# Kernel tuning notes

Hardware: AMD Instinct MI355X
Metric: run time of the kernel (lower is better)

The kernel has to match this reference:

```python
import jax, jax.numpy as jnp
import numpy as np

B, S, HID, H = 2, 2048, 1024, 16
D = HID // H  # head dim = 64


def setup_inputs() -> dict:
    key = jax.random.key(0)
    ks = jax.random.split(key, 16)
    scale = 0.02
    inp = {
        "hidden_states": jax.random.normal(ks[0], (B, S, HID), jnp.float32),
        "attention_mask": jnp.zeros((B, 1, 1, S), jnp.float32),
        "hashtag_mask": jax.random.uniform(ks[1], (B, S), jnp.float32),
        "mention_mask": jax.random.uniform(ks[2], (B, S), jnp.float32),
        "emoji_mask": jax.random.uniform(ks[3], (B, S), jnp.float32),
        # Linear weights stored as [in, out] (torch uses [out, in]; math identical via x @ W)
        "Wq": jax.random.normal(ks[4], (HID, HID), jnp.float32) * scale,
        "bq": jnp.zeros((HID,), jnp.float32),
        "Wk": jax.random.normal(ks[5], (HID, HID), jnp.float32) * scale,
        "bk": jnp.zeros((HID,), jnp.float32),
        "Wv": jax.random.normal(ks[6], (HID, HID), jnp.float32) * scale,
        "bv": jnp.zeros((HID,), jnp.float32),
        "Wo": jax.random.normal(ks[7], (HID, HID), jnp.float32) * scale,
        "bo": jnp.zeros((HID,), jnp.float32),
        # per-head scalar social biases [1, H, 1, 1]
        "hashtag_bias": jax.random.normal(ks[8], (1, H, 1, 1), jnp.float32) * 0.1,
        "mention_bias": jax.random.normal(ks[9], (1, H, 1, 1), jnp.float32) * 0.1,
        "emoji_bias": jax.random.normal(ks[10], (1, H, 1, 1), jnp.float32) * 0.1,
    }
    return inp


def _split_heads(x):
    # [B, S, HID] -> [B, H, S, D]
    b, s, _ = x.shape
    return x.reshape(b, s, H, D).transpose(0, 2, 1, 3)


def reference(hidden_states, attention_mask, hashtag_mask, mention_mask, emoji_mask,
              Wq, bq, Wk, bk, Wv, bv, Wo, bo,
              hashtag_bias, mention_bias, emoji_bias):
    q = _split_heads(hidden_states @ Wq + bq)  # [B,H,S,D]
    k = _split_heads(hidden_states @ Wk + bk)
    v = _split_heads(hidden_states @ Wv + bv)

    scores = jnp.einsum("bhqd,bhkd->bhqk", q, k) / jnp.sqrt(jnp.float32(D))
    # social token biases: mask [B,S] -> [B,1,1,S], broadcast over query axis
    scores = scores + hashtag_bias * hashtag_mask[:, None, None, :]
    scores = scores + mention_bias * mention_mask[:, None, None, :]
    scores = scores + emoji_bias * emoji_mask[:, None, None, :]
    scores = scores + attention_mask

    probs = jax.nn.softmax(scores, axis=-1)  # dropout is identity in eval
    ctx = jnp.einsum("bhqk,bhkd->bhqd", probs, v)  # [B,H,S,D]
    ctx = ctx.transpose(0, 2, 1, 3).reshape(hidden_states.shape[0], hidden_states.shape[1], HID)
    out = ctx @ Wo + bo
    return out, probs
```

## Files before the change

### kernel.cpp

```cpp
#include <hip/hip_runtime.h>
#include <hip/hip_bf16.h>

typedef __hip_bfloat16 bf16;
typedef short short8 __attribute__((ext_vector_type(8)));
typedef float f32x4 __attribute__((ext_vector_type(4)));

#define B_ 2
#define S_ 2048
#define HID_ 1024
#define H_ 16
#define D_ 64
#define M_ (B_*S_)

__device__ __forceinline__ void gload16(const bf16* g, bf16* l) {
    __builtin_amdgcn_global_load_lds(
        (const __attribute__((address_space(1))) unsigned int*)g,
        (__attribute__((address_space(3))) unsigned int*)l, 16, 0, 0);
}

__device__ __forceinline__ f32x4 mfma16(short8 a, short8 b, f32x4 c) {
    return __builtin_amdgcn_mfma_f32_16x16x32_bf16(a, b, c, 0, 0, 0);
}


__global__ void k_convert_x(const float* __restrict__ in, bf16* __restrict__ out, int n) {
    int i = blockIdx.x * blockDim.x + threadIdx.x;
    if (i * 4 < n) {
        float4 v = ((const float4*)in)[i];
        out[i*4+0] = __float2bfloat16(v.x);
        out[i*4+1] = __float2bfloat16(v.y);
        out[i*4+2] = __float2bfloat16(v.z);
        out[i*4+3] = __float2bfloat16(v.w);
    }
}

__global__ void k_trans_w(const float* W0, const float* W1, const float* W2, const float* W3,
                          bf16* T0, bf16* T1, bf16* T2, bf16* T3) {
    const float* W = blockIdx.z==0 ? W0 : blockIdx.z==1 ? W1 : blockIdx.z==2 ? W2 : W3;
    bf16*       T = blockIdx.z==0 ? T0 : blockIdx.z==1 ? T1 : blockIdx.z==2 ? T2 : T3;
    __shared__ float tile[32][33];
    int tx = threadIdx.x, ty = threadIdx.y;
    int k0 = blockIdx.x * 32, n0 = blockIdx.y * 32;
#pragma unroll
    for (int j = 0; j < 4; j++)
        tile[ty + j*8][tx] = W[(size_t)(k0 + ty + j*8) * HID_ + n0 + tx];
    __syncthreads();
#pragma unroll
    for (int j = 0; j < 4; j++)
        T[(size_t)(n0 + ty + j*8) * HID_ + k0 + tx] = __float2bfloat16(tile[tx][ty + j*8]);
}

__global__ void k_keybias(const float* __restrict__ am, const float* __restrict__ hm,
                          const float* __restrict__ mm, const float* __restrict__ em,
                          const float* __restrict__ hb, const float* __restrict__ mb,
                          const float* __restrict__ eb, float* __restrict__ kb) {
    int i = blockIdx.x * blockDim.x + threadIdx.x;
    int kk = i & (S_ - 1);
    int bh = i >> 11;
    int h = bh & (H_ - 1);
    int b = bh >> 4;
    int bk = b * S_ + kk;
    kb[i] = am[bk] + hb[h]*hm[bk] + mb[h]*mm[bk] + eb[h]*em[bk];
}

__global__ void k_trans_v(const bf16* __restrict__ v, bf16* __restrict__ vT) {
    __shared__ bf16 tile[32][33];
    int bh = blockIdx.z;
    int s0 = blockIdx.x * 32, d0 = blockIdx.y * 32;
    int tx = threadIdx.x, ty = threadIdx.y;
    const bf16* vb = v + (size_t)bh * S_ * D_;
    bf16* vTb = vT + (size_t)bh * D_ * S_;
#pragma unroll
    for (int j = 0; j < 4; j++)
        tile[ty + j*8][tx] = vb[(size_t)(s0 + ty + j*8) * D_ + d0 + tx];
    __syncthreads();
#pragma unroll
    for (int j = 0; j < 4; j++)
        vTb[(size_t)(d0 + ty + j*8) * S_ + s0 + tx] = tile[tx][ty + j*8];
}

template<bool SPLIT>
__global__ __launch_bounds__(256) void k_gemm(
    const bf16* __restrict__ A,
    const bf16* __restrict__ Bt0, const bf16* __restrict__ Bt1, const bf16* __restrict__ Bt2,
    const float* __restrict__ bi0, const float* __restrict__ bi1, const float* __restrict__ bi2,
    bf16* d0, bf16* d1, bf16* d2, float* dF)
{
    const int K = HID_;
    int z = blockIdx.z;
    const bf16* Bt = (z==0) ? Bt0 : (z==1 ? Bt1 : Bt2);
    const float* bias = (z==0) ? bi0 : (z==1 ? bi1 : bi2);
    bf16* dst = (z==0) ? d0 : (z==1 ? d1 : d2);
    float scale = (SPLIT && z==0) ? 0.125f : 1.0f;

    __shared__ bf16 As[128*32];
    __shared__ bf16 Bs[128*32];
    int t = threadIdx.x;
    int lane = t & 63, wave = t >> 6;
    int wm = wave >> 1, wn = wave & 1;
    int bm = blockIdx.y * 128, bn = blockIdx.x * 128;

    f32x4 acc[4][4];
#pragma unroll
    for (int i = 0; i < 4; i++)
#pragma unroll
        for (int j = 0; j < 4; j++) acc[i][j] = f32x4{0.f, 0.f, 0.f, 0.f};

    const bf16* aG = A  + (size_t)(bm + (t >> 2)) * K + (t & 3) * 8;
    const bf16* bG = Bt + (size_t)(bn + (t >> 2)) * K + (t & 3) * 8;
    bf16* asD = As + t * 8;
    bf16* bsD = Bs + t * 8;
    int r16 = lane & 15, kq = (lane >> 4) * 8;

    for (int k0 = 0; k0 < K; k0 += 32) {
        __syncthreads();
        gload16(aG + k0,          asD);
        gload16(aG + 64*K + k0,   asD + 2048);
        gload16(bG + k0,          bsD);
        gload16(bG + 64*K + k0,   bsD + 2048);
        __syncthreads();
        short8 af[4], bfv[4];
#pragma unroll
        for (int mt = 0; mt < 4; mt++)
            af[mt] = *(const short8*)(As + (wm*64 + mt*16 + r16) * 32 + kq);
#pragma unroll
        for (int nt = 0; nt < 4; nt++)
            bfv[nt] = *(const short8*)(Bs + (wn*64 + nt*16 + r16) * 32 + kq);
#pragma unroll
        for (int mt = 0; mt < 4; mt++)
#pragma unroll
            for (int nt = 0; nt < 4; nt++)
                acc[mt][nt] = mfma16(af[mt], bfv[nt], acc[mt][nt]);
    }

    int quad = lane >> 4;
#pragma unroll
    for (int mt = 0; mt < 4; mt++) {
#pragma unroll
        for (int nt = 0; nt < 4; nt++) {
            int c = bn + wn*64 + nt*16 + r16;
            int rbase = bm + wm*64 + mt*16 + quad*4;
            float bv = bias[c];
#pragma unroll
            for (int r = 0; r < 4; r++) {
                int m = rbase + r;
                float v = acc[mt][nt][r] + bv;
                if constexpr (SPLIT) {
                    v *= scale;
                    int bb = m >> 11, ss = m & 2047, hh = c >> 6, dd = c & 63;
                    dst[(((size_t)bb * H_ + hh) * S_ + ss) * D_ + dd] = __float2bfloat16(v);
                } else {
                    dF[(size_t)m * HID_ + c] = v;
                }
            }
        }
    }
}

__global__ __launch_bounds__(256) void k_attn(
    const bf16* __restrict__ q, const bf16* __restrict__ k,
    const bf16* __restrict__ vT, const float* __restrict__ keyBias,
    float* __restrict__ probs, bf16* __restrict__ ctx)
{
    __shared__ bf16 Ps[4][16][152];
    int t = threadIdx.x, lane = t & 63, w = t >> 6;
    int l16 = lane & 15, quad = lane >> 4;
    int bh = blockIdx.y, qt = blockIdx.x;
    int qrow = qt * 64 + w * 16;

    const bf16* qp = q + ((size_t)bh * S_ + qrow + l16) * D_ + quad * 8;
    short8 qf0 = *(const short8*)qp;
    short8 qf1 = *(const short8*)(qp + 32);

    const bf16* kb_ = k + (size_t)bh * S_ * D_;
    const float* kbias = keyBias + bh * S_;

    float rm[4], rl[4];
#pragma unroll
    for (int r = 0; r < 4; r++) { rm[r] = -1e30f; rl[r] = 0.f; }

    for (int kt = 0; kt < 128; ++kt) {
        int key = kt * 16;
        const bf16* kp = kb_ + (size_t)(key + l16) * D_ + quad * 8;
        short8 kv0 = *(const short8*)kp;
        short8 kv1 = *(const short8*)(kp + 32);
        f32x4 s = f32x4{0.f, 0.f, 0.f, 0.f};
        s = mfma16(qf0, kv0, s);
        s = mfma16(qf1, kv1, s);
        float bias = kbias[key + l16];
#pragma unroll
        for (int r = 0; r < 4; r++) {
            float sv = s[r] + bias;
            float mn = fmaxf(rm[r], sv);
            rl[r] = rl[r] * __expf(rm[r] - mn) + __expf(sv - mn);
            rm[r] = mn;
        }
    }
#pragma unroll
    for (int off = 1; off < 16; off <<= 1) {
#pragma unroll
        for (int r = 0; r < 4; r++) {
            float mo = __shfl_xor(rm[r], off);
            float lo = __shfl_xor(rl[r], off);
            float mn = fmaxf(rm[r], mo);
            rl[r] = rl[r] * __expf(rm[r] - mn) + lo * __expf(mo - mn);
            rm[r] = mn;
        }
    }
    float invl[4];
#pragma unroll
    for (int r = 0; r < 4; r++) invl[r] = 1.f / rl[r];

    f32x4 o[4];
#pragma unroll
    for (int r = 0; r < 4; r++) o[r] = f32x4{0.f, 0.f, 0.f, 0.f};
    const bf16* vb = vT + (size_t)bh * D_ * S_;
    float* pr = probs + (size_t)bh * S_ * S_;

    for (int c = 0; c < 16; ++c) {
        int keyc = c * 128;
#pragma unroll
        for (int nt = 0; nt < 8; ++nt) {
            int key = keyc + nt * 16;
            const bf16* kp = kb_ + (size_t)(key + l16) * D_ + quad * 8;
            short8 kv0 = *(const short8*)kp;
            short8 kv1 = *(const short8*)(kp + 32);
            f32x4 s = f32x4{0.f, 0.f, 0.f, 0.f};
            s = mfma16(qf0, kv0, s);
            s = mfma16(qf1, kv1, s);
            float bias = kbias[key + l16];
#pragma unroll
            for (int r = 0; r < 4; r++) {
                float p = __expf(s[r] + bias - rm[r]) * invl[r];
                pr[(size_t)(qrow + quad*4 + r) * S_ + key + l16] = p;
                Ps[w][quad*4 + r][nt*16 + l16] = __float2bfloat16(p);
            }
        }
#pragma unroll
        for (int ks = 0; ks < 4; ++ks) {
            short8 pa = *(const short8*)&Ps[w][l16][ks*32 + quad*8];
#pragma unroll
            for (int dt = 0; dt < 4; ++dt) {
                const bf16* vp = vb + (size_t)(dt*16 + l16) * S_ + keyc + ks*32 + quad*8;
                short8 vv = *(const short8*)vp;
                o[dt] = mfma16(pa, vv, o[dt]);
            }
        }
    }

    int b = bh >> 4, h = bh & 15;
#pragma unroll
    for (int dt = 0; dt < 4; dt++) {
#pragma unroll
        for (int r = 0; r < 4; r++) {
            int ss = qrow + quad*4 + r;
            int dd = dt*16 + l16;
            ctx[((size_t)b * S_ + ss) * HID_ + h * D_ + dd] = __float2bfloat16(o[dt][r]);
        }
    }
}


extern "C" void kernel_launch(void* const* d_in, const int* in_sizes, int n_in,
                              void* d_out, int out_size, void* d_ws, size_t ws_size,
                              hipStream_t stream) {
    (void)in_sizes; (void)n_in; (void)out_size; (void)ws_size;
    const float* hidden = (const float*)d_in[0];
    const float* amask  = (const float*)d_in[1];
    const float* hmask  = (const float*)d_in[2];
    const float* mmask  = (const float*)d_in[3];
    const float* emask  = (const float*)d_in[4];
    const float* Wq = (const float*)d_in[5];  const float* bq = (const float*)d_in[6];
    const float* Wk = (const float*)d_in[7];  const float* bk = (const float*)d_in[8];
    const float* Wv = (const float*)d_in[9];  const float* bv = (const float*)d_in[10];
    const float* Wo = (const float*)d_in[11]; const float* bo = (const float*)d_in[12];
    const float* hb = (const float*)d_in[13];
    const float* mb = (const float*)d_in[14];
    const float* eb = (const float*)d_in[15];

    char* ws = (char*)d_ws;
    bf16* X    = (bf16*)(ws + 0);
    bf16* Wtq  = (bf16*)(ws + 8388608);
    bf16* Wtk  = (bf16*)(ws + 10485760);
    bf16* Wtv  = (bf16*)(ws + 12582912);
    bf16* Wto  = (bf16*)(ws + 14680064);
    bf16* qw   = (bf16*)(ws + 16777216);
    bf16* kw   = (bf16*)(ws + 25165824);
    bf16* vw   = (bf16*)(ws + 33554432);
    bf16* vTw  = (bf16*)(ws + 41943040);
    bf16* ctx  = (bf16*)(ws + 50331648);
    float* kbias = (float*)(ws + 58720256);

    float* out   = (float*)d_out;
    float* probs = out + (size_t)B_ * S_ * HID_;

    k_convert_x<<<4096, 256, 0, stream>>>(hidden, X, B_ * S_ * HID_);
    dim3 tb(32, 8);
    k_trans_w<<<dim3(32, 32, 4), tb, 0, stream>>>(Wq, Wk, Wv, Wo, Wtq, Wtk, Wtv, Wto);
    k_keybias<<<256, 256, 0, stream>>>(amask, hmask, mmask, emask, hb, mb, eb, kbias);
    k_gemm<true><<<dim3(8, 32, 3), 256, 0, stream>>>(X, Wtq, Wtk, Wtv, bq, bk, bv,
                                                     qw, kw, vw, nullptr);
    k_trans_v<<<dim3(64, 2, 32), tb, 0, stream>>>(vw, vTw);
    k_attn<<<dim3(32, 32), 256, 0, stream>>>(qw, kw, vTw, kbias, probs, ctx);
    k_gemm<false><<<dim3(8, 32, 1), 256, 0, stream>>>(ctx, Wto, Wto, Wto, bo, bo, bo,
                                                      nullptr, nullptr, nullptr, out);
}
```

Before: 1.060 ms.

## Split attention keys across warps and keep scores in registers

The attention kernel now gives each block 16 query rows and has its four warps each take a quarter of the keys, instead of each warp owning 16 rows and scanning all keys twice. Scores for the warp's 512 keys are computed once and held in 32 register fragments, which removes the second QK^T pass and the online-softmax rescaling. Row max and sum are combined across warps through shared memory, and the partial PV outputs are summed in shared memory before warp 0 writes ctx. This launches four times as many blocks but adds heavy register pressure (128 floats of scores per lane), extra block barriers, and a cross-warp output reduction.

```diff
diff --git a/kernel.cpp b/kernel.cpp
--- a/kernel.cpp
+++ b/kernel.cpp
@@ -162,11 +162,17 @@
     const bf16* __restrict__ vT, const float* __restrict__ keyBias,
     float* __restrict__ probs, bf16* __restrict__ ctx)
 {
-    __shared__ bf16 Ps[4][16][152];
+    __shared__ __align__(16) char smraw[4 * 16 * 152 * sizeof(bf16)];
+    bf16  (*Ps)[16][152] = (bf16 (*)[16][152])smraw;
+    float (*Oc)[16][68]  = (float (*)[16][68])smraw;
+    __shared__ float redm[4][16];
+    __shared__ float reds[4][16];
+
     int t = threadIdx.x, lane = t & 63, w = t >> 6;
     int l16 = lane & 15, quad = lane >> 4;
     int bh = blockIdx.y, qt = blockIdx.x;
-    int qrow = qt * 64 + w * 16;
+    int qrow = qt * 16;
+    int key0 = w * 512;
 
     const bf16* qp = q + ((size_t)bh * S_ + qrow + l16) * D_ + quad * 8;
     short8 qf0 = *(const short8*)qp;
@@ -175,63 +181,88 @@
     const bf16* kb_ = k + (size_t)bh * S_ * D_;
     const float* kbias = keyBias + bh * S_;
 
-    float rm[4], rl[4];
-#pragma unroll
-    for (int r = 0; r < 4; r++) { rm[r] = -1e30f; rl[r] = 0.f; }
-
-    for (int kt = 0; kt < 128; ++kt) {
-        int key = kt * 16;
+    f32x4 s[32];
+#pragma unroll
+    for (int kt = 0; kt < 32; ++kt) {
+        int key = key0 + kt * 16;
         const bf16* kp = kb_ + (size_t)(key + l16) * D_ + quad * 8;
         short8 kv0 = *(const short8*)kp;
         short8 kv1 = *(const short8*)(kp + 32);
-        f32x4 s = f32x4{0.f, 0.f, 0.f, 0.f};
-        s = mfma16(qf0, kv0, s);
-        s = mfma16(qf1, kv1, s);
-        float bias = kbias[key + l16];
-#pragma unroll
-        for (int r = 0; r < 4; r++) {
-            float sv = s[r] + bias;
-            float mn = fmaxf(rm[r], sv);
-            rl[r] = rl[r] * __expf(rm[r] - mn) + __expf(sv - mn);
-            rm[r] = mn;
-        }
-    }
-#pragma unroll
-    for (int off = 1; off < 16; off <<= 1) {
-#pragma unroll
-        for (int r = 0; r < 4; r++) {
-            float mo = __shfl_xor(rm[r], off);
-            float lo = __shfl_xor(rl[r], off);
-            float mn = fmaxf(rm[r], mo);
-            rl[r] = rl[r] * __expf(rm[r] - mn) + lo * __expf(mo - mn);
-            rm[r] = mn;
-        }
-    }
+        f32x4 acc = f32x4{0.f, 0.f, 0.f, 0.f};
+        acc = mfma16(qf0, kv0, acc);
+        acc = mfma16(qf1, kv1, acc);
+        s[kt] = acc;
+    }
+#pragma unroll
+    for (int kt = 0; kt < 32; ++kt) {
+        float b = kbias[key0 + kt * 16 + l16];
+#pragma unroll
+        for (int r = 0; r < 4; ++r) s[kt][r] += b;
+    }
+
+    float rm[4];
+#pragma unroll
+    for (int r = 0; r < 4; ++r) rm[r] = s[0][r];
+#pragma unroll
+    for (int kt = 1; kt < 32; ++kt)
+#pragma unroll
+        for (int r = 0; r < 4; ++r) rm[r] = fmaxf(rm[r], s[kt][r]);
+#pragma unroll
+    for (int off = 1; off < 16; off <<= 1)
+#pragma unroll
+        for (int r = 0; r < 4; ++r) rm[r] = fmaxf(rm[r], __shfl_xor(rm[r], off));
+    if (l16 == 0) {
+#pragma unroll
+        for (int r = 0; r < 4; ++r) redm[w][quad*4 + r] = rm[r];
+    }
+    __syncthreads();
+#pragma unroll
+    for (int r = 0; r < 4; ++r) {
+        float m = fmaxf(fmaxf(redm[0][quad*4+r], redm[1][quad*4+r]),
+                        fmaxf(redm[2][quad*4+r], redm[3][quad*4+r]));
+        rm[r] = m;
+    }
+
+    float rl[4] = {0.f, 0.f, 0.f, 0.f};
+#pragma unroll
+    for (int kt = 0; kt < 32; ++kt)
+#pragma unroll
+        for (int r = 0; r < 4; ++r) {
+            float p = __expf(s[kt][r] - rm[r]);
+            s[kt][r] = p;
+            rl[r] += p;
+        }
+#pragma unroll
+    for (int off = 1; off < 16; off <<= 1)
+#pragma unroll
+        for (int r = 0; r < 4; ++r) rl[r] += __shfl_xor(rl[r], off);
+    if (l16 == 0) {
+#pragma unroll
+        for (int r = 0; r < 4; ++r) reds[w][quad*4 + r] = rl[r];
+    }
+    __syncthreads();
     float invl[4];
 #pragma unroll
-    for (int r = 0; r < 4; r++) invl[r] = 1.f / rl[r];
+    for (int r = 0; r < 4; ++r) {
+        float l = reds[0][quad*4+r] + reds[1][quad*4+r] + reds[2][quad*4+r] + reds[3][quad*4+r];
+        invl[r] = 1.f / l;
+    }
 
     f32x4 o[4];
 #pragma unroll
-    for (int r = 0; r < 4; r++) o[r] = f32x4{0.f, 0.f, 0.f, 0.f};
+    for (int r = 0; r < 4; ++r) o[r] = f32x4{0.f, 0.f, 0.f, 0.f};
     const bf16* vb = vT + (size_t)bh * D_ * S_;
     float* pr = probs + (size_t)bh * S_ * S_;
 
-    for (int c = 0; c < 16; ++c) {
-        int keyc = c * 128;
+    for (int c = 0; c < 4; ++c) {
+        int keyc = key0 + c * 128;
 #pragma unroll
         for (int nt = 0; nt < 8; ++nt) {
+            int kt = c * 8 + nt;
             int key = keyc + nt * 16;
-            const bf16* kp = kb_ + (size_t)(key + l16) * D_ + quad * 8;
-            short8 kv0 = *(const short8*)kp;
-            short8 kv1 = *(const short8*)(kp + 32);
-            f32x4 s = f32x4{0.f, 0.f, 0.f, 0.f};
-            s = mfma16(qf0, kv0, s);
-            s = mfma16(qf1, kv1, s);
-            float bias = kbias[key + l16];
-#pragma unroll
-            for (int r = 0; r < 4; r++) {
-                float p = __expf(s[r] + bias - rm[r]) * invl[r];
+#pragma unroll
+            for (int r = 0; r < 4; ++r) {
+                float p = s[kt][r] * invl[r];
                 pr[(size_t)(qrow + quad*4 + r) * S_ + key + l16] = p;
                 Ps[w][quad*4 + r][nt*16 + l16] = __float2bfloat16(p);
             }
@@ -248,14 +279,27 @@
         }
     }
 
-    int b = bh >> 4, h = bh & 15;
-#pragma unroll
-    for (int dt = 0; dt < 4; dt++) {
-#pragma unroll
-        for (int r = 0; r < 4; r++) {
-            int ss = qrow + quad*4 + r;
-            int dd = dt*16 + l16;
-            ctx[((size_t)b * S_ + ss) * HID_ + h * D_ + dd] = __float2bfloat16(o[dt][r]);
+    __syncthreads();
+    if (w > 0) {
+#pragma unroll
+        for (int dt = 0; dt < 4; ++dt)
+#pragma unroll
+            for (int r = 0; r < 4; ++r)
+                Oc[w-1][quad*4 + r][dt*16 + l16] = o[dt][r];
+    }
+    __syncthreads();
+    if (w == 0) {
+        int b = bh >> 4, h = bh & 15;
+#pragma unroll
+        for (int dt = 0; dt < 4; ++dt) {
+#pragma unroll
+            for (int r = 0; r < 4; ++r) {
+                float v = o[dt][r] + Oc[0][quad*4+r][dt*16+l16]
+                        + Oc[1][quad*4+r][dt*16+l16] + Oc[2][quad*4+r][dt*16+l16];
+                int ss = qrow + quad*4 + r;
+                int dd = dt*16 + l16;
+                ctx[((size_t)b * S_ + ss) * HID_ + h * D_ + dd] = __float2bfloat16(v);
+            }
         }
     }
 }
@@ -301,7 +345,7 @@
     k_gemm<true><<<dim3(8, 32, 3), 256, 0, stream>>>(X, Wtq, Wtk, Wtv, bq, bk, bv,
                                                      qw, kw, vw, nullptr);
     k_trans_v<<<dim3(64, 2, 32), tb, 0, stream>>>(vw, vTw);
-    k_attn<<<dim3(32, 32), 256, 0, stream>>>(qw, kw, vTw, kbias, probs, ctx);
+    k_attn<<<dim3(128, 32), 256, 0, stream>>>(qw, kw, vTw, kbias, probs, ctx);
     k_gemm<false><<<dim3(8, 32, 1), 256, 0, stream>>>(ctx, Wto, Wto, Wto, bo, bo, bo,
                                                       nullptr, nullptr, nullptr, out);
 }
```

Measured after the change: 976.3 us. 1.09x faster.
